# Kernel tuning notes

Hardware: AMD Instinct MI355X
Metric: run time of the kernel (lower is better)

## Reference

```python
import jax, jax.numpy as jnp
import numpy as np

HEADS = 12
HEAD_DIM = 64          # dim_out // heads = 768 // 12
Q_STRIDE = 4
WINDOW_SIZE = 16       # post-pool tokens per window; pre-pool = Q_STRIDE*WINDOW_SIZE = 64
DIM = 768
DIM_OUT = 768


def setup_inputs() -> dict:
    key = jax.random.key(0)
    k1, k2, k3 = jax.random.split(key, 3)
    B, N = 32, 3136
    x = jax.random.normal(k1, (B, N, DIM), dtype=jnp.float32)
    Wqkv = jax.random.normal(k2, (DIM, 3 * DIM_OUT), dtype=jnp.float32) * 0.02
    bqkv = jnp.zeros((3 * DIM_OUT,), dtype=jnp.float32)
    Wproj = jax.random.normal(k3, (DIM_OUT, DIM_OUT), dtype=jnp.float32) * 0.02
    bproj = jnp.zeros((DIM_OUT,), dtype=jnp.float32)
    return {"x": x, "Wqkv": Wqkv, "bqkv": bqkv, "Wproj": Wproj, "bproj": bproj}


def reference(x, Wqkv, bqkv, Wproj, bproj):
    B, N, _ = x.shape
    num_windows = N // (Q_STRIDE * WINDOW_SIZE)  # 49
    scale = HEAD_DIM ** (-0.5)

    # QKV projection (torch Linear uses x @ W^T; here Wqkv is stored [dim, 3*dim_out])
    qkv = x @ Wqkv + bqkv                                  # [B, N, 3*dim_out]
    # Same reshape as torch: windows are the inner split of the token axis
    qkv = qkv.reshape(B, N // num_windows, num_windows, 3, HEADS, HEAD_DIM)
    qkv = jnp.transpose(qkv, (3, 0, 4, 2, 1, 5))           # [3, B, h, w, t, d]
    q, k, v = qkv[0], qkv[1], qkv[2]                       # t = Q_STRIDE*WINDOW_SIZE

    # Query max-pooling over stride groups
    q = q.reshape(B, HEADS, num_windows, Q_STRIDE, WINDOW_SIZE, HEAD_DIM).max(axis=3)
    # q: [B, h, w, WINDOW_SIZE, d]

    # Scaled dot-product attention within each window
    logits = jnp.einsum('bhwqd,bhwkd->bhwqk', q, k) * scale
    attn = jax.nn.softmax(logits, axis=-1)
    o = jnp.einsum('bhwqk,bhwkd->bhwqd', attn, v)          # [B, h, w, q, d]

    # transpose(1,3) then flatten tokens, channels = heads*head_dim
    o = jnp.transpose(o, (0, 3, 2, 1, 4)).reshape(B, -1, DIM_OUT)
    return o @ Wproj + bproj
```

## Files before the change

kernel.cpp:

```cpp
#include <hip/hip_runtime.h>
#include <hip/hip_bf16.h>


typedef __bf16 bf16x8 __attribute__((ext_vector_type(8)));
typedef float f32x4 __attribute__((ext_vector_type(4)));
typedef unsigned short u16x8 __attribute__((ext_vector_type(8)));

#define GLOBAL_AS __attribute__((address_space(1)))
#define LDS_AS __attribute__((address_space(3)))

__device__ __forceinline__ unsigned short f2bf(float f) {
    unsigned u = __builtin_bit_cast(unsigned, f);
    u += 0x7FFFu + ((u >> 16) & 1u);
    return (unsigned short)(u >> 16);
}
__device__ __forceinline__ float bf2f(unsigned short h) {
    return __builtin_bit_cast(float, (unsigned)h << 16);
}

__device__ __forceinline__ void load16_to_lds(const void* g, void* l) {
    __builtin_amdgcn_global_load_lds((const GLOBAL_AS unsigned int*)g,
                                     (LDS_AS unsigned int*)l, 16, 0, 0);
}

__global__ __launch_bounds__(256)
void cvt_f32_bf16(const float* __restrict__ in,
                  unsigned short* __restrict__ out, long n8) {
    const long i = (long)blockIdx.x * blockDim.x + threadIdx.x;
    if (i >= n8) return;
    float4 f0 = ((const float4*)in)[i * 2];
    float4 f1 = ((const float4*)in)[i * 2 + 1];
    uint4 o;
    o.x = (unsigned)f2bf(f0.x) | ((unsigned)f2bf(f0.y) << 16);
    o.y = (unsigned)f2bf(f0.z) | ((unsigned)f2bf(f0.w) << 16);
    o.z = (unsigned)f2bf(f1.x) | ((unsigned)f2bf(f1.y) << 16);
    o.w = (unsigned)f2bf(f1.z) | ((unsigned)f2bf(f1.w) << 16);
    ((uint4*)out)[i] = o;
}

__global__ void transpose_cvt2(const float* __restrict__ W0,
                               unsigned short* __restrict__ T0,
                               const float* __restrict__ W1,
                               unsigned short* __restrict__ T1) {
    __shared__ float tile[32][33];
    int bxi = blockIdx.x;
    const float* W; unsigned short* Wt; int N;
    if (bxi < 72) { W = W0; Wt = T0; N = 2304; }
    else          { W = W1; Wt = T1; N = 768; bxi -= 72; }
    const int K = 768;
    int bx = bxi * 32;
    int by = blockIdx.y * 32;
    int tx = threadIdx.x & 31, ty = threadIdx.x >> 5;
    #pragma unroll
    for (int i = 0; i < 32; i += 8)
        tile[ty + i][tx] = W[(size_t)(by + ty + i) * N + bx + tx];
    __syncthreads();
    #pragma unroll
    for (int i = 0; i < 32; i += 8)
        Wt[(size_t)(bx + ty + i) * K + by + tx] = f2bf(tile[tx][ty + i]);
}

#define VM_WAIT3 asm volatile("s_waitcnt vmcnt(3)" ::: "memory")
#define VM_WAIT2 asm volatile("s_waitcnt vmcnt(2)" ::: "memory")
#define VM_WAIT0 asm volatile("s_waitcnt vmcnt(0)" ::: "memory")

#define GPHASE(BUF, CSW, IH, LOADBG, STG, WAITS) do {                        \
    if (LOADBG) {                                                            \
        const unsigned short* bb = &ls[(BUF) * 32768 + 16384 + (CSW)];       \
        bg[0] = *(const bf16x8*)&bb[(wn +  0 + lane15) * 64];                \
        bg[1] = *(const bf16x8*)&bb[(wn + 16 + lane15) * 64];                \
        bg[2] = *(const bf16x8*)&bb[(wn + 32 + lane15) * 64];                \
        bg[3] = *(const bf16x8*)&bb[(wn + 48 + lane15) * 64];                \
    }                                                                        \
    {                                                                        \
        const unsigned short* ab = &ls[(BUF) * 32768 + (CSW)];               \
        af[0] = *(const bf16x8*)&ab[(wm + (IH)*64 +  0 + lane15) * 64];      \
        af[1] = *(const bf16x8*)&ab[(wm + (IH)*64 + 16 + lane15) * 64];      \
        af[2] = *(const bf16x8*)&ab[(wm + (IH)*64 + 32 + lane15) * 64];      \
        af[3] = *(const bf16x8*)&ab[(wm + (IH)*64 + 48 + lane15) * 64];      \
    }                                                                        \
    STG;                                                                     \
    WAITS;                                                                   \
    __builtin_amdgcn_s_barrier();                                            \
    asm volatile("s_waitcnt lgkmcnt(0)" ::: "memory");                       \
    __builtin_amdgcn_sched_barrier(0);                                       \
    __builtin_amdgcn_s_setprio(1);                                           \
    _Pragma("unroll")                                                        \
    for (int ii = 0; ii < 4; ++ii)                                           \
        _Pragma("unroll")                                                    \
        for (int j = 0; j < 4; ++j)                                          \
            acc[(IH)*4 + ii][j] = __builtin_amdgcn_mfma_f32_16x16x32_bf16(   \
                bg[j], af[ii], acc[(IH)*4 + ii][j], 0, 0, 0);                \
    __builtin_amdgcn_s_setprio(0);                                           \
    __builtin_amdgcn_s_barrier();                                            \
} while (0)

template <bool QKV>
__global__ __launch_bounds__(512, 2)
void gemm_bt256(const unsigned short* __restrict__ A,
                const unsigned short* __restrict__ Bt,
                const float* __restrict__ bias,
                void* __restrict__ Cv, int N, int K) {
    __shared__ alignas(16) unsigned short ls[65536];

    const int tid  = threadIdx.x;
    const int lane = tid & 63;
    const int wave = tid >> 6;
    const int wm = (wave >> 2) * 128;
    const int wn = (wave & 3) * 64;
    const int lane15 = lane & 15;
    const int quad   = lane >> 4;
    const int csw0 = ((quad    ) ^ (lane & 7)) * 8;
    const int csw1 = ((quad + 4) ^ (lane & 7)) * 8;

    const int nwg = (int)(gridDim.x * gridDim.y);
    const int hid = (int)(blockIdx.y * gridDim.x + blockIdx.x);
    const int q8  = nwg >> 3, r8 = nwg & 7;
    const int xcd = hid & 7;
    const int lid = (xcd < r8 ? xcd * (q8 + 1) : r8 * (q8 + 1) + (xcd - r8) * q8)
                    + (hid >> 3);
    const int tileX = lid % (int)gridDim.x;
    const int tileY = lid / (int)gridDim.x;
    const long bm = (long)tileY * 256;
    const long bn = (long)tileX * 256;

    const int r0 = tid >> 3;
    const int lc = (tid & 7) ^ (r0 & 7);
    const unsigned short* gAq[4];
    #pragma unroll
    for (int q = 0; q < 4; ++q) {
        const int mq = (int)bm + q * 64 + r0;
        long srow;
        if constexpr (QKV) {
            const int b  = mq / 3136;
            const int r3 = mq - b * 3136;
            srow = (long)b * 3136 + (long)(r3 & 63) * 49 + (r3 >> 6);
        } else {
            srow = mq;
        }
        gAq[q] = A + srow * (long)K + lc * 8;
    }
    const unsigned short* gB = Bt + (bn + r0) * (long)K + lc * 8;
    const int ldsWaveBase = wave * 512;

    auto STAGE_A = [&](int buf, int q, int kt) {
        load16_to_lds(gAq[q] + kt * 64,
                      &ls[buf * 32768 + q * 4096 + ldsWaveBase]);
    };
    auto STAGE_B = [&](int buf, int q, int kt) {
        load16_to_lds(gB + (long)q * 64 * K + kt * 64,
                      &ls[buf * 32768 + 16384 + q * 4096 + ldsWaveBase]);
    };

    f32x4 acc[8][4] = {};
    bf16x8 af[4], bg[4];

    const int NT = K >> 6;
    const int NI = NT >> 1;

    STAGE_A(0, 0, 0); STAGE_A(0, 1, 0); STAGE_A(0, 2, 0); STAGE_A(0, 3, 0);
    STAGE_B(0, 0, 0); STAGE_B(0, 1, 0); STAGE_B(0, 2, 0); STAGE_B(0, 3, 0);
    STAGE_A(1, 0, 1); STAGE_A(1, 2, 1);
    VM_WAIT2;
    __builtin_amdgcn_s_barrier();

    for (int i = 0; i < NI; ++i) {
        const int t2 = 2 * i;
        const bool last = (i == NI - 1);
        GPHASE(0, csw0, 0, 1,
               { STAGE_A(1, 1, t2 + 1); STAGE_A(1, 3, t2 + 1); STAGE_B(1, 0, t2 + 1); },
               { (void)0; });
        GPHASE(0, csw0, 1, 0,
               { STAGE_B(1, 1, t2 + 1); STAGE_B(1, 2, t2 + 1); STAGE_B(1, 3, t2 + 1); },
               { (void)0; });
        GPHASE(0, csw1, 0, 1, { (void)0; }, { (void)0; });
        GPHASE(0, csw1, 1, 0,
               { if (!last) { STAGE_B(0, 0, t2 + 2); STAGE_B(0, 1, t2 + 2);
                              STAGE_B(0, 2, t2 + 2); } },
               { if (last) { VM_WAIT0; } else { VM_WAIT3; } });
        GPHASE(1, csw0, 0, 1,
               { if (!last) { STAGE_B(0, 3, t2 + 2); STAGE_A(0, 0, t2 + 2);
                              STAGE_A(0, 2, t2 + 2); } },
               { (void)0; });
        GPHASE(1, csw0, 1, 0,
               { if (!last) { STAGE_A(0, 1, t2 + 2); STAGE_A(0, 3, t2 + 2); } },
               { (void)0; });
        GPHASE(1, csw1, 0, 1, { (void)0; }, { (void)0; });
        GPHASE(1, csw1, 1, 0,
               { if (!last) { STAGE_A(1, 0, t2 + 3); STAGE_A(1, 2, t2 + 3); VM_WAIT2; } },
               { (void)0; });
    }

    const int rbase = (int)(bm) + wm + lane15;
    if constexpr (QKV) {
        const int colBase = (int)bn + wn;
        const int sec = colBase / 768;
        const int hh  = (colBase - sec * 768) >> 6;
        const long shOff = (long)sec * 49152 + hh * 4096 + quad * 4;
        unsigned short* qout = (unsigned short*)Cv;
        float4 bv[4];
        #pragma unroll
        for (int j = 0; j < 4; ++j)
            bv[j] = *(const float4*)&bias[colBase + quad * 4 + j * 16];
        #pragma unroll
        for (int i = 0; i < 8; ++i) {
            const int m  = rbase + i * 16;
            const int b  = m / 3136;
            const int r3 = m - b * 3136;
            unsigned short* rp = qout + (long)(b * 49 + (r3 >> 6)) * 147456
                                      + shOff + (long)(r3 & 63) * 64;
            #pragma unroll
            for (int j = 0; j < 4; ++j) {
                ushort4 s;
                s.x = f2bf(acc[i][j][0] + bv[j].x);
                s.y = f2bf(acc[i][j][1] + bv[j].y);
                s.z = f2bf(acc[i][j][2] + bv[j].z);
                s.w = f2bf(acc[i][j][3] + bv[j].w);
                *(ushort4*)(rp + j * 16) = s;
            }
        }
    } else {
        const int cbase = (int)bn + wn + quad * 4;
        #pragma unroll
        for (int j = 0; j < 4; ++j) {
            const int col = cbase + j * 16;
            const float4 bv = *(const float4*)&bias[col];
            #pragma unroll
            for (int i = 0; i < 8; ++i) {
                const long row = (long)rbase + i * 16;
                const size_t idx = (size_t)row * N + col;
                float4 s;
                s.x = acc[i][j][0] + bv.x;
                s.y = acc[i][j][1] + bv.y;
                s.z = acc[i][j][2] + bv.z;
                s.w = acc[i][j][3] + bv.w;
                *(float4*)((float*)Cv + idx) = s;
            }
        }
    }
}

__global__ __launch_bounds__(256, 4)
void attn_win_mfma(const unsigned short* __restrict__ qkv,
                   unsigned short* __restrict__ o) {
    const int hg = blockIdx.x;
    const int w  = blockIdx.y;
    const int b  = blockIdx.z;
    const int wave = threadIdx.x >> 6;
    const int lane = threadIdx.x & 63;
    const int h = hg * 4 + wave;
    const int l = lane & 15;
    const int quad = lane >> 4;

    __shared__ alignas(16) unsigned short vT[4][64 * 64];
    __shared__ alignas(16) unsigned short ps[4][16 * 64];

    const long slab = (long)(b * 49 + w) * 147456;
    const long hOff = (long)h * 4096;

    bf16x8 af[2];
    {
        const unsigned short* qr = qkv + slab + hOff + (long)l * 64 + quad * 8;
        float m0[8], m1[8];
        #pragma unroll
        for (int sg = 0; sg < 4; ++sg) {
            uint4 u0 = *(const uint4*)(qr + sg * 1024);
            uint4 u1 = *(const uint4*)(qr + sg * 1024 + 32);
            const unsigned short* p0 = (const unsigned short*)&u0;
            const unsigned short* p1 = (const unsigned short*)&u1;
            #pragma unroll
            for (int e = 0; e < 8; ++e) {
                float f0 = bf2f(p0[e]), f1 = bf2f(p1[e]);
                if (sg == 0) { m0[e] = f0; m1[e] = f1; }
                else { m0[e] = fmaxf(m0[e], f0); m1[e] = fmaxf(m1[e], f1); }
            }
        }
        u16x8 a0, a1;
        #pragma unroll
        for (int e = 0; e < 8; ++e) {
            a0[e] = f2bf(m0[e] * 0.125f);
            a1[e] = f2bf(m1[e] * 0.125f);
        }
        af[0] = __builtin_bit_cast(bf16x8, a0);
        af[1] = __builtin_bit_cast(bf16x8, a1);
    }

    {
        const unsigned short* vr = qkv + slab + 98304 + hOff + (long)lane * 64;
        unsigned short* vw = &vT[wave][0];
        const int ch = lane >> 3, le = lane & 7;
        #pragma unroll
        for (int i = 0; i < 8; ++i) {
            uint4 u = *(const uint4*)(vr + i * 8);
            const unsigned short* pe = (const unsigned short*)&u;
            #pragma unroll
            for (int e = 0; e < 8; ++e) {
                const int d = i * 8 + e;
                vw[d * 64 + ((ch ^ (d & 7)) << 3) + le] = pe[e];
            }
        }
    }

    f32x4 Sc[4] = {};
    {
        bf16x8 bk0, bk1;
        __builtin_amdgcn_s_setprio(1);
        #pragma unroll
        for (int tt = 0; tt < 4; ++tt) {
            const unsigned short* kr =
                qkv + slab + 49152 + hOff + (long)(tt * 16 + l) * 64 + quad * 8;
            bk0 = __builtin_bit_cast(bf16x8, *(const uint4*)kr);
            bk1 = __builtin_bit_cast(bf16x8, *(const uint4*)(kr + 32));
            Sc[tt] = __builtin_amdgcn_mfma_f32_16x16x32_bf16(af[0], bk0, Sc[tt], 0, 0, 0);
            Sc[tt] = __builtin_amdgcn_mfma_f32_16x16x32_bf16(af[1], bk1, Sc[tt], 0, 0, 0);
        }
        __builtin_amdgcn_s_setprio(0);
    }

    float pr[4][4];
    {
        #pragma unroll
        for (int r = 0; r < 4; ++r) {
            float mx = fmaxf(fmaxf(Sc[0][r], Sc[1][r]), fmaxf(Sc[2][r], Sc[3][r]));
            #pragma unroll
            for (int off = 1; off < 16; off <<= 1)
                mx = fmaxf(mx, __shfl_xor(mx, off));
            float sum = 0.f;
            #pragma unroll
            for (int tt = 0; tt < 4; ++tt) {
                pr[tt][r] = __expf(Sc[tt][r] - mx);
                sum += pr[tt][r];
            }
            #pragma unroll
            for (int off = 1; off < 16; off <<= 1)
                sum += __shfl_xor(sum, off);
            const float inv = 1.0f / sum;
            #pragma unroll
            for (int tt = 0; tt < 4; ++tt) pr[tt][r] *= inv;
        }
    }

    {
        unsigned short* pw = &ps[wave][0];
        #pragma unroll
        for (int r = 0; r < 4; ++r) {
            const int row = quad * 4 + r;
            #pragma unroll
            for (int tt = 0; tt < 4; ++tt) {
                const int c = (tt << 1) + (l >> 3);
                pw[row * 64 + ((c ^ (row & 7)) << 3) + (l & 7)] = f2bf(pr[tt][r]);
            }
        }
    }

    f32x4 Oc[4] = {};
    {
        __builtin_amdgcn_s_setprio(1);
        #pragma unroll
        for (int s = 0; s < 2; ++s) {
            const int csw = (((s << 2) + quad) ^ (l & 7)) << 3;
            bf16x8 ap = *(const bf16x8*)&ps[wave][l * 64 + csw];
            #pragma unroll
            for (int tt = 0; tt < 4; ++tt) {
                bf16x8 bv = *(const bf16x8*)&vT[wave][(tt * 16 + l) * 64 + csw];
                Oc[tt] = __builtin_amdgcn_mfma_f32_16x16x32_bf16(ap, bv, Oc[tt], 0, 0, 0);
            }
        }
        __builtin_amdgcn_s_setprio(0);
    }

    {
        const long obase = ((long)b * 784 + (long)(quad * 4) * 49 + w) * 768 + h * 64 + l;
        #pragma unroll
        for (int tt = 0; tt < 4; ++tt)
            #pragma unroll
            for (int r = 0; r < 4; ++r)
                o[obase + (long)r * 49 * 768 + tt * 16] = f2bf(Oc[tt][r]);
    }
}

extern "C" void kernel_launch(void* const* d_in, const int* in_sizes, int n_in,
                              void* d_out, int out_size, void* d_ws, size_t ws_size,
                              hipStream_t stream) {
    const float* x     = (const float*)d_in[0];
    const float* Wqkv  = (const float*)d_in[1];
    const float* bqkv  = (const float*)d_in[2];
    const float* Wproj = (const float*)d_in[3];
    const float* bproj = (const float*)d_in[4];
    float* out = (float*)d_out;

    const long needed1 = (32L * 3136 * 768 + 32L * 3136 * 2304 +
                          25088L * 768 + 2304L * 768 + 768L * 768) * 2;
    const int C  = (ws_size >= (size_t)needed1) ? 1 : 4;
    const int CB = 32 / C;
    const long XC = (long)CB * 3136 * 768;
    const long QC = (long)CB * 3136 * 2304;

    char* p = (char*)d_ws;
    unsigned short* xb    = (unsigned short*)p; p += XC * 2;
    unsigned short* qkvb  = (unsigned short*)p; p += QC * 2;
    unsigned short* ob    = (unsigned short*)p; p += 25088L * 768 * 2;
    unsigned short* WqkvT = (unsigned short*)p; p += 2304L * 768 * 2;
    unsigned short* WprojT= (unsigned short*)p; p += 768L * 768 * 2;

    transpose_cvt2<<<dim3(96, 24), 256, 0, stream>>>(Wqkv, WqkvT, Wproj, WprojT);

    const int M = CB * 3136;
    for (int c = 0; c < C; ++c) {
        cvt_f32_bf16<<<(int)((M * 96L + 255) / 256), 256, 0, stream>>>(
            x + (size_t)c * XC, xb, M * 96L);
        gemm_bt256<true><<<dim3(9, M / 256), 512, 0, stream>>>(
            xb, WqkvT, bqkv, qkvb, 2304, 768);
        attn_win_mfma<<<dim3(3, 49, CB), 256, 0, stream>>>(
            qkvb, ob + (size_t)c * CB * 784 * 768);
    }
    gemm_bt256<false><<<dim3(3, 98), 512, 0, stream>>>(
        ob, WprojT, bproj, out, 768, 768);
}
```

Measured before the change: 1.059 ms.

## Fuse fp32-to-bf16 conversion of x into QKV GEMM A-tile loading

```diff
diff --git a/kernel.cpp b/kernel.cpp
--- a/kernel.cpp
+++ b/kernel.cpp
@@ -4,7 +4,6 @@
 
 typedef __bf16 bf16x8 __attribute__((ext_vector_type(8)));
 typedef float f32x4 __attribute__((ext_vector_type(4)));
-typedef unsigned short u16x8 __attribute__((ext_vector_type(8)));
 
 #define GLOBAL_AS __attribute__((address_space(1)))
 #define LDS_AS __attribute__((address_space(3)))
@@ -14,6 +13,10 @@
     u += 0x7FFFu + ((u >> 16) & 1u);
     return (unsigned short)(u >> 16);
 }
+__device__ __forceinline__ unsigned f2bf_u(unsigned u) {
+    u += 0x7FFFu + ((u >> 16) & 1u);
+    return u >> 16;
+}
 __device__ __forceinline__ float bf2f(unsigned short h) {
     return __builtin_bit_cast(float, (unsigned)h << 16);
 }
@@ -21,21 +24,6 @@
 __device__ __forceinline__ void load16_to_lds(const void* g, void* l) {
     __builtin_amdgcn_global_load_lds((const GLOBAL_AS unsigned int*)g,
                                      (LDS_AS unsigned int*)l, 16, 0, 0);
-}
-
-__global__ __launch_bounds__(256)
-void cvt_f32_bf16(const float* __restrict__ in,
-                  unsigned short* __restrict__ out, long n8) {
-    const long i = (long)blockIdx.x * blockDim.x + threadIdx.x;
-    if (i >= n8) return;
-    float4 f0 = ((const float4*)in)[i * 2];
-    float4 f1 = ((const float4*)in)[i * 2 + 1];
-    uint4 o;
-    o.x = (unsigned)f2bf(f0.x) | ((unsigned)f2bf(f0.y) << 16);
-    o.y = (unsigned)f2bf(f0.z) | ((unsigned)f2bf(f0.w) << 16);
-    o.z = (unsigned)f2bf(f1.x) | ((unsigned)f2bf(f1.y) << 16);
-    o.w = (unsigned)f2bf(f1.z) | ((unsigned)f2bf(f1.w) << 16);
-    ((uint4*)out)[i] = o;
 }
 
 __global__ void transpose_cvt2(const float* __restrict__ W0,
@@ -60,9 +48,11 @@
         Wt[(size_t)(bx + ty + i) * K + by + tx] = f2bf(tile[tx][ty + i]);
 }
 
-#define VM_WAIT3 asm volatile("s_waitcnt vmcnt(3)" ::: "memory")
-#define VM_WAIT2 asm volatile("s_waitcnt vmcnt(2)" ::: "memory")
-#define VM_WAIT0 asm volatile("s_waitcnt vmcnt(0)" ::: "memory")
+#define VM_WAIT12 asm volatile("s_waitcnt vmcnt(12)" ::: "memory")
+#define VM_WAIT4  asm volatile("s_waitcnt vmcnt(4)" ::: "memory")
+#define VM_WAIT3  asm volatile("s_waitcnt vmcnt(3)" ::: "memory")
+#define VM_WAIT2  asm volatile("s_waitcnt vmcnt(2)" ::: "memory")
+#define VM_WAIT0  asm volatile("s_waitcnt vmcnt(0)" ::: "memory")
 
 #define GPHASE(BUF, CSW, IH, LOADBG, STG, WAITS) do {                        \
     if (LOADBG) {                                                            \
@@ -95,9 +85,30 @@
     __builtin_amdgcn_s_barrier();                                            \
 } while (0)
 
+#define ISSUE_A(AR, KT) do {                                                 \
+    _Pragma("unroll")                                                        \
+    for (int q = 0; q < 4; ++q) {                                            \
+        const float* sp = gAqF[q] + (long)(KT) * 64;                         \
+        AR[q][0] = *(const uint4*)sp;                                        \
+        AR[q][1] = *(const uint4*)(sp + 4);                                  \
+    }                                                                        \
+} while (0)
+
+#define WRITE_A(BUF, AR) do {                                                \
+    _Pragma("unroll")                                                        \
+    for (int q = 0; q < 4; ++q) {                                            \
+        uint4 wv;                                                            \
+        wv.x = f2bf_u(AR[q][0].x) | (f2bf_u(AR[q][0].y) << 16);              \
+        wv.y = f2bf_u(AR[q][0].z) | (f2bf_u(AR[q][0].w) << 16);              \
+        wv.z = f2bf_u(AR[q][1].x) | (f2bf_u(AR[q][1].y) << 16);              \
+        wv.w = f2bf_u(AR[q][1].z) | (f2bf_u(AR[q][1].w) << 16);              \
+        *(uint4*)&ls[(BUF) * 32768 + q * 4096 + ldsWaveBase + lane * 8] = wv;\
+    }                                                                        \
+} while (0)
+
 template <bool QKV>
 __global__ __launch_bounds__(512, 2)
-void gemm_bt256(const unsigned short* __restrict__ A,
+void gemm_bt256(const void* __restrict__ Av,
                 const unsigned short* __restrict__ Bt,
                 const float* __restrict__ bias,
                 void* __restrict__ Cv, int N, int K) {
@@ -126,22 +137,23 @@
 
     const int r0 = tid >> 3;
     const int lc = (tid & 7) ^ (r0 & 7);
+    const int ldsWaveBase = wave * 512;
+
+    const float* gAqF[4];
     const unsigned short* gAq[4];
     #pragma unroll
     for (int q = 0; q < 4; ++q) {
         const int mq = (int)bm + q * 64 + r0;
-        long srow;
         if constexpr (QKV) {
             const int b  = mq / 3136;
             const int r3 = mq - b * 3136;
-            srow = (long)b * 3136 + (long)(r3 & 63) * 49 + (r3 >> 6);
+            const long srow = (long)b * 3136 + (long)(r3 & 63) * 49 + (r3 >> 6);
+            gAqF[q] = (const float*)Av + srow * 768 + lc * 8;
         } else {
-            srow = mq;
-        }
-        gAq[q] = A + srow * (long)K + lc * 8;
+            gAq[q] = (const unsigned short*)Av + (long)mq * K + lc * 8;
+        }
     }
     const unsigned short* gB = Bt + (bn + r0) * (long)K + lc * 8;
-    const int ldsWaveBase = wave * 512;
 
     auto STAGE_A = [&](int buf, int q, int kt) {
         load16_to_lds(gAq[q] + kt * 64,
@@ -158,37 +170,72 @@
     const int NT = K >> 6;
     const int NI = NT >> 1;
 
-    STAGE_A(0, 0, 0); STAGE_A(0, 1, 0); STAGE_A(0, 2, 0); STAGE_A(0, 3, 0);
-    STAGE_B(0, 0, 0); STAGE_B(0, 1, 0); STAGE_B(0, 2, 0); STAGE_B(0, 3, 0);
-    STAGE_A(1, 0, 1); STAGE_A(1, 2, 1);
-    VM_WAIT2;
-    __builtin_amdgcn_s_barrier();
-
-    for (int i = 0; i < NI; ++i) {
-        const int t2 = 2 * i;
-        const bool last = (i == NI - 1);
-        GPHASE(0, csw0, 0, 1,
-               { STAGE_A(1, 1, t2 + 1); STAGE_A(1, 3, t2 + 1); STAGE_B(1, 0, t2 + 1); },
-               { (void)0; });
-        GPHASE(0, csw0, 1, 0,
-               { STAGE_B(1, 1, t2 + 1); STAGE_B(1, 2, t2 + 1); STAGE_B(1, 3, t2 + 1); },
-               { (void)0; });
-        GPHASE(0, csw1, 0, 1, { (void)0; }, { (void)0; });
-        GPHASE(0, csw1, 1, 0,
-               { if (!last) { STAGE_B(0, 0, t2 + 2); STAGE_B(0, 1, t2 + 2);
-                              STAGE_B(0, 2, t2 + 2); } },
-               { if (last) { VM_WAIT0; } else { VM_WAIT3; } });
-        GPHASE(1, csw0, 0, 1,
-               { if (!last) { STAGE_B(0, 3, t2 + 2); STAGE_A(0, 0, t2 + 2);
-                              STAGE_A(0, 2, t2 + 2); } },
-               { (void)0; });
-        GPHASE(1, csw0, 1, 0,
-               { if (!last) { STAGE_A(0, 1, t2 + 2); STAGE_A(0, 3, t2 + 2); } },
-               { (void)0; });
-        GPHASE(1, csw1, 0, 1, { (void)0; }, { (void)0; });
-        GPHASE(1, csw1, 1, 0,
-               { if (!last) { STAGE_A(1, 0, t2 + 3); STAGE_A(1, 2, t2 + 3); VM_WAIT2; } },
-               { (void)0; });
+    if constexpr (QKV) {
+        uint4 arE[4][2], arO[4][2];
+        ISSUE_A(arE, 0);
+        WRITE_A(0, arE);
+        STAGE_B(0, 0, 0); STAGE_B(0, 1, 0); STAGE_B(0, 2, 0); STAGE_B(0, 3, 0);
+        ISSUE_A(arO, 1);
+        STAGE_B(1, 0, 1); STAGE_B(1, 1, 1); STAGE_B(1, 2, 1); STAGE_B(1, 3, 1);
+        VM_WAIT12;
+        __builtin_amdgcn_s_barrier();
+
+        for (int i = 0; i < NI; ++i) {
+            const int t2  = 2 * i;
+            const int ka2 = (t2 + 2 < NT) ? t2 + 2 : NT - 1;
+            const int ka3 = (t2 + 3 < NT) ? t2 + 3 : NT - 1;
+            GPHASE(0, csw0, 0, 1,
+                   { VM_WAIT4; WRITE_A(1, arO); ISSUE_A(arE, ka2); },
+                   { (void)0; });
+            GPHASE(0, csw0, 1, 0, { (void)0; }, { (void)0; });
+            GPHASE(0, csw1, 0, 1, { (void)0; }, { (void)0; });
+            GPHASE(0, csw1, 1, 0,
+                   { STAGE_B(0, 0, ka2); STAGE_B(0, 1, ka2);
+                     STAGE_B(0, 2, ka2); STAGE_B(0, 3, ka2); VM_WAIT12; },
+                   { (void)0; });
+            GPHASE(1, csw0, 0, 1,
+                   { VM_WAIT4; WRITE_A(0, arE); ISSUE_A(arO, ka3); },
+                   { (void)0; });
+            GPHASE(1, csw0, 1, 0, { (void)0; }, { (void)0; });
+            GPHASE(1, csw1, 0, 1, { (void)0; }, { (void)0; });
+            GPHASE(1, csw1, 1, 0,
+                   { STAGE_B(1, 0, ka3); STAGE_B(1, 1, ka3);
+                     STAGE_B(1, 2, ka3); STAGE_B(1, 3, ka3); VM_WAIT12; },
+                   { (void)0; });
+        }
+    } else {
+        STAGE_A(0, 0, 0); STAGE_A(0, 1, 0); STAGE_A(0, 2, 0); STAGE_A(0, 3, 0);
+        STAGE_B(0, 0, 0); STAGE_B(0, 1, 0); STAGE_B(0, 2, 0); STAGE_B(0, 3, 0);
+        STAGE_A(1, 0, 1); STAGE_A(1, 2, 1);
+        VM_WAIT2;
+        __builtin_amdgcn_s_barrier();
+
+        for (int i = 0; i < NI; ++i) {
+            const int t2 = 2 * i;
+            const bool last = (i == NI - 1);
+            GPHASE(0, csw0, 0, 1,
+                   { STAGE_A(1, 1, t2 + 1); STAGE_A(1, 3, t2 + 1); STAGE_B(1, 0, t2 + 1); },
+                   { (void)0; });
+            GPHASE(0, csw0, 1, 0,
+                   { STAGE_B(1, 1, t2 + 1); STAGE_B(1, 2, t2 + 1); STAGE_B(1, 3, t2 + 1); },
+                   { (void)0; });
+            GPHASE(0, csw1, 0, 1, { (void)0; }, { (void)0; });
+            GPHASE(0, csw1, 1, 0,
+                   { if (!last) { STAGE_B(0, 0, t2 + 2); STAGE_B(0, 1, t2 + 2);
+                                  STAGE_B(0, 2, t2 + 2); } },
+                   { if (last) { VM_WAIT0; } else { VM_WAIT3; } });
+            GPHASE(1, csw0, 0, 1,
+                   { if (!last) { STAGE_B(0, 3, t2 + 2); STAGE_A(0, 0, t2 + 2);
+                                  STAGE_A(0, 2, t2 + 2); } },
+                   { (void)0; });
+            GPHASE(1, csw0, 1, 0,
+                   { if (!last) { STAGE_A(0, 1, t2 + 2); STAGE_A(0, 3, t2 + 2); } },
+                   { (void)0; });
+            GPHASE(1, csw1, 0, 1, { (void)0; }, { (void)0; });
+            GPHASE(1, csw1, 1, 0,
+                   { if (!last) { STAGE_A(1, 0, t2 + 3); STAGE_A(1, 2, t2 + 3); VM_WAIT2; } },
+                   { (void)0; });
+        }
     }
 
     const int rbase = (int)(bm) + wm + lane15;
@@ -275,14 +322,14 @@
                 else { m0[e] = fmaxf(m0[e], f0); m1[e] = fmaxf(m1[e], f1); }
             }
         }
-        u16x8 a0, a1;
+        unsigned short a0[8], a1[8];
         #pragma unroll
         for (int e = 0; e < 8; ++e) {
             a0[e] = f2bf(m0[e] * 0.125f);
             a1[e] = f2bf(m1[e] * 0.125f);
         }
-        af[0] = __builtin_bit_cast(bf16x8, a0);
-        af[1] = __builtin_bit_cast(bf16x8, a1);
+        af[0] = __builtin_bit_cast(bf16x8, *(uint4*)a0);
+        af[1] = __builtin_bit_cast(bf16x8, *(uint4*)a1);
     }
 
     {
@@ -389,15 +436,13 @@
     const float* bproj = (const float*)d_in[4];
     float* out = (float*)d_out;
 
-    const long needed1 = (32L * 3136 * 768 + 32L * 3136 * 2304 +
+    const long needed1 = (32L * 3136 * 2304 +
                           25088L * 768 + 2304L * 768 + 768L * 768) * 2;
     const int C  = (ws_size >= (size_t)needed1) ? 1 : 4;
     const int CB = 32 / C;
-    const long XC = (long)CB * 3136 * 768;
     const long QC = (long)CB * 3136 * 2304;
 
     char* p = (char*)d_ws;
-    unsigned short* xb    = (unsigned short*)p; p += XC * 2;
     unsigned short* qkvb  = (unsigned short*)p; p += QC * 2;
     unsigned short* ob    = (unsigned short*)p; p += 25088L * 768 * 2;
     unsigned short* WqkvT = (unsigned short*)p; p += 2304L * 768 * 2;
@@ -407,10 +452,8 @@
 
     const int M = CB * 3136;
     for (int c = 0; c < C; ++c) {
-        cvt_f32_bf16<<<(int)((M * 96L + 255) / 256), 256, 0, stream>>>(
-            x + (size_t)c * XC, xb, M * 96L);
         gemm_bt256<true><<<dim3(9, M / 256), 512, 0, stream>>>(
-            xb, WqkvT, bqkv, qkvb, 2304, 768);
+            x + (size_t)c * M * 768, WqkvT, bqkv, qkvb, 2304, 768);
         attn_win_mfma<<<dim3(3, 49, CB), 256, 0, stream>>>(
             qkvb, ob + (size_t)c * CB * 784 * 768);
     }
```

Result: slower. 1.853 ms (+74.9%).
